# Kernel tuning notes

Hardware: AMD Instinct MI355X
Metric: run time of the kernel (lower is better)

Reference implementation:

```python
import jax, jax.numpy as jnp
import numpy as np

D_EMBED = 384
D_FF = 64
TAU = 0.1
T0, T1 = 0.0, 1.0
N_STEPS = 10


def setup_inputs() -> dict:
    key = jax.random.key(0)
    ks = jax.random.split(key, 6)
    B, n, d, f = 64, 1024, D_EMBED, D_FF
    init = lambda k, sh, fan: (jax.random.normal(k, sh, jnp.float32) / np.sqrt(fan)).astype(jnp.float32)
    return {
        "embeddings": jax.random.normal(ks[0], (B, n, d), jnp.float32),
        "W1": init(ks[1], (d + 1, f), d + 1), "b1": jnp.zeros((f,), jnp.float32),
        "W2": init(ks[2], (f, f), f),       "b2": jnp.zeros((f,), jnp.float32),
        "W3": init(ks[3], (f, d), f),       "b3": jnp.zeros((d,), jnp.float32),
        "Ws": init(ks[4], (d, 1), d),       "bs": jnp.zeros((1,), jnp.float32),
    }


def reference(embeddings, W1, b1, W2, b2, W3, b3, Ws, bs):
    B, n, d = embeddings.shape
    h0 = embeddings.reshape(B * n, d)
    dt = (T1 - T0) / N_STEPS

    def ode_f(t, h):
        # time-aware dynamics: concat scalar t to hidden state
        t_col = jnp.full((h.shape[0], 1), t, dtype=h.dtype)
        x = jnp.concatenate([h, t_col], axis=-1)
        x = jnp.tanh(x @ W1 + b1)
        x = jnp.tanh(x @ W2 + b2)
        return x @ W3 + b3

    def rk4_step(h, t):
        k1 = ode_f(t, h)
        k2 = ode_f(t + dt * 0.5, h + (dt * 0.5) * k1)
        k3 = ode_f(t + dt * 0.5, h + (dt * 0.5) * k2)
        k4 = ode_f(t + dt, h + dt * k3)
        return h + (dt / 6.0) * (k1 + 2.0 * k2 + 2.0 * k3 + k4), None

    ts = T0 + dt * jnp.arange(N_STEPS, dtype=jnp.float32)
    h_final, _ = jax.lax.scan(rk4_step, h0, ts)
    h_final = h_final.reshape(B, n, d)

    scores = (h_final @ Ws + bs).squeeze(-1)  # (B, n)

    # NeuralSort (Grover et al.): P_hat = softmax((C - A@1@1^T)^T / tau)
    s_col = scores[:, :, None]                        # (B, n, 1)
    A = jnp.abs(s_col - scores[:, None, :])           # (B, n, n) pairwise |s_i - s_j|
    row_sum = jnp.sum(A, axis=-1, keepdims=True)      # A @ one one^T, broadcast over cols
    scaling = (n + 1 - 2.0 * (jnp.arange(n, dtype=scores.dtype) + 1.0))  # (n,)
    C = s_col * scaling[None, None, :]                # C[b,i,j] = s_i * scaling_j
    P_max = jnp.transpose(C - row_sum, (0, 2, 1))
    P_hat = jax.nn.softmax(P_max / TAU, axis=-1)      # (B, n, n) soft permutation

    x_sorted = jnp.einsum('bij,bjd->bid', P_hat, embeddings)
    return x_sorted, scores
```

## Files before the change

### kernel.cpp

```cpp
#include <hip/hip_runtime.h>
#include <hip/hip_bf16.h>

#define NT 1024
#define DD 384
#define FF 64

typedef __attribute__((ext_vector_type(8))) _Float16 half8;
typedef __attribute__((ext_vector_type(4))) float f32x4;
typedef __attribute__((ext_vector_type(4))) unsigned uint32x4;

#define LO_SCALE 2048.f
#define INV2048  4.8828125e-4f

__device__ __forceinline__ float tanh_fast(float x){
    x = fminf(fmaxf(x, -15.f), 15.f);
    float e = __expf(2.f*x);
    return (e - 1.f) * __builtin_amdgcn_rcpf(e + 1.f);
}

__device__ __forceinline__ unsigned short h2u(_Float16 h){ return __builtin_bit_cast(unsigned short, h); }

__device__ __forceinline__ unsigned short split2_comp(float x, int comp){
    _Float16 hi = (_Float16)x;
    if (comp == 0) return h2u(hi);
    float r = (x - (float)hi) * LO_SCALE;
    _Float16 lo = (_Float16)r;
    return h2u(lo);
}

__device__ __forceinline__ void split_pack4(const float* v, unsigned* ph, unsigned* pl){
#pragma unroll
    for (int p=0;p<2;++p){
        float a=v[2*p], b=v[2*p+1];
        _Float16 ha=(_Float16)a, hb=(_Float16)b;
        ph[p] = (unsigned)h2u(ha) | ((unsigned)h2u(hb)<<16);
        float ra=(a-(float)ha)*LO_SCALE, rb=(b-(float)hb)*LO_SCALE;
        pl[p] = __builtin_bit_cast(unsigned, __builtin_amdgcn_cvt_pkrtz(ra, rb));
    }
}

__global__ void k_prep(const float* __restrict__ W1, const float* __restrict__ W2,
                       const float* __restrict__ W3, unsigned short* __restrict__ F)
{
    unsigned short* W1F = F;
    unsigned short* W2F = F + 49152;
    unsigned short* W3F = F + 57344;
    const int t = blockIdx.x*256 + threadIdx.x;
    const int NTH = gridDim.x*256;
    for (int i=t; i<49152; i+=NTH){
        int j=i&7, l=(i>>3)&63, u=i>>9;
        int kb=u%12, v=u/12, mb=v&3, comp=v>>2;
        int k=kb*32+8*(l>>4)+j, c=mb*16+(l&15);
        W1F[i] = split2_comp(W1[k*64+c], comp);
    }
    for (int i=t; i<8192; i+=NTH){
        int j=i&7, l=(i>>3)&63, u=i>>9;
        int kb=u&1, v=u>>1, mb=v&3, comp=v>>2;
        int k=kb*32+8*(l>>4)+j, c=mb*16+(l&15);
        W2F[i] = split2_comp(W2[k*64+c], comp);
    }
    for (int i=t; i<49152; i+=NTH){
        int j=i&7, l=(i>>3)&63, u=i>>9;
        int kb=u&1, v=u>>1, mb=v%24, comp=v/24;
        int k=kb*32+8*(l>>4)+j, c=mb*16+(l&15);
        W3F[i] = split2_comp(W3[k*384+c], comp);
    }
}

__global__ void k_prepE(const float* __restrict__ emb, unsigned short* __restrict__ EF)
{
    __shared__ float tile[32][388];
    const int b   = blockIdx.x >> 5;
    const int kb  = blockIdx.x & 31;
    const int tid = threadIdx.x;
    const float* src = emb + ((long long)b*NT + kb*32)*DD;
    for (int o = tid; o < 32*96; o += 256){
        int r = o/96, c4 = (o%96)*4;
        *(float4*)&tile[r][c4] = *(const float4*)&src[r*384 + c4];
    }
    __syncthreads();
    unsigned short* dst = EF + ((long long)b*24*32 + kb)*512;
    for (int o = tid; o < 24*512; o += 256){
        int mb = o >> 9, q = o & 511;
        int l = q >> 3, jj = q & 7;
        float v = tile[8*(l>>4)+jj][mb*16 + (l&15)];
        dst[(long long)mb*16384 + q] = h2u((_Float16)v);
    }
}

#define MFMA3(AH,AL,BH,BL,ACC,ACC2) do{ \
    ACC  = __builtin_amdgcn_mfma_f32_16x16x32_f16(AH,BH,ACC,0,0,0); \
    ACC2 = __builtin_amdgcn_mfma_f32_16x16x32_f16(AH,BL,ACC2,0,0,0); \
    ACC2 = __builtin_amdgcn_mfma_f32_16x16x32_f16(AL,BH,ACC2,0,0,0); \
}while(0)

struct AF { half8 h, l; };
#define LDA(P, CS) AF{ *(const half8*)(P), *(const half8*)((P)+(CS)) }
#define LDB(BASE, KB) do{ \
    bh = *(const half8*)((BASE) + (KB)*2048); \
    bl = *(const half8*)((BASE) + (KB)*2048 + 1024); \
}while(0)

__global__ __launch_bounds__(512) __attribute__((amdgpu_waves_per_eu(2,2)))
void k_ode(const float* __restrict__ emb,
           const float* __restrict__ W1,
           const float* __restrict__ b1, const float* __restrict__ b2,
           const float* __restrict__ b3, const float* __restrict__ Ws,
           const float* __restrict__ bs,
           const unsigned short* __restrict__ W1F,
           const unsigned short* __restrict__ W2F,
           const unsigned short* __restrict__ W3F,
           float* __restrict__ scores)
{
    extern __shared__ char smem[];
    unsigned short* hf  = (unsigned short*)smem;
    unsigned short* x1f = hf  + 24576;
    unsigned short* x2f = x1f + 4096;
    float*          red = (float*)(x2f + 4096);
    float*          h0l = red + 512;

    unsigned* hf32  = (unsigned*)hf;
    unsigned* x1f32 = (unsigned*)x1f;
    unsigned* x2f32 = (unsigned*)x2f;

    const int tid  = threadIdx.x;
    const int lane = tid & 63;
    const int w    = __builtin_amdgcn_readfirstlane(tid >> 6);
    const int g    = lane >> 4;
    const int rr   = lane & 15;
    const int nb   = w & 1;
    const int mbA  = w >> 1;
    const int rowl = nb*16 + rr;
    const long long row0 = (long long)blockIdx.x * 32;
    const float dt = 0.1f;

    const unsigned short* hrd  = hf  + nb*512 + lane*8;
    const unsigned short* x1rd = x1f + nb*512 + lane*8;
    const unsigned short* x2rd = x2f + nb*512 + lane*8;
    const unsigned wxp = nb*256 + rr*4 + 2*(g&1);
    const unsigned wx1 = ((unsigned)(mbA>>1))*1024 + 64u*((2*mbA+(g>>1))&3) + wxp;
    const int h0base = rowl*388 + mbA*96 + 4*g;

    float arc[24];
#pragma unroll
    for (int t=0;t<6;++t){
        f32x4 v = *(const f32x4*)(emb + (row0+rowl)*DD + mbA*96 + t*16 + 4*g);
        float hw[4] = {v[0],v[1],v[2],v[3]};
        *(float4*)(h0l + h0base + 16*t) = make_float4(hw[0],hw[1],hw[2],hw[3]);
        unsigned ph[2],pl[2];
        split_pack4(hw,ph,pl);
        const unsigned wh = ((unsigned)((6*mbA+t)>>1))*1024 + 64u*((2*t+(g>>1))&3) + wxp;
        *(uint2*)(hf32 + wh       ) = make_uint2(ph[0],ph[1]);
        *(uint2*)(hf32 + wh +  512) = make_uint2(pl[0],pl[1]);
    }

#define M3SEC(T, ACC, ACC2) do{ \
    ACC2 = (f32x4){0.f,0.f,0.f,0.f}; \
    const unsigned short* A3 = W3F + (unsigned)((6*mbA+(T))*2)*512 + lane*8; \
    AF w0 = LDA(A3, 24576); \
    AF w1 = LDA(A3+512, 24576); \
    MFMA3(w0.h,w0.l,B0h,B0l,ACC,ACC2); \
    MFMA3(w1.h,w1.l,B1h,B1l,ACC,ACC2); \
    __builtin_amdgcn_sched_barrier(0); \
}while(0)

#define M3UPD(T, ACC, ACC2) do{ \
    f32x4 h0v = *(const f32x4*)(h0l + h0base + 16*(T)); \
    float hw[4]; \
    if (stage < 3){ \
        _Pragma("unroll") \
        for (int r=0;r<4;++r){ float kr=fmaf(ACC2[r], INV2048, ACC[r]); \
            arc[4*(T)+r] = fmaf(wacc, kr, arc[4*(T)+r]); \
            hw[r] = fmaf(cs, kr, h0v[r]); } \
    } else { \
        _Pragma("unroll") \
        for (int r=0;r<4;++r){ float kr=fmaf(ACC2[r], INV2048, ACC[r]); \
            arc[4*(T)+r] = fmaf(wacc, kr, arc[4*(T)+r]); \
            hw[r] = h0v[r] + arc[4*(T)+r]; } \
        *(float4*)(h0l + h0base + 16*(T)) = make_float4(hw[0],hw[1],hw[2],hw[3]); \
    } \
    unsigned ph[2],pl[2]; \
    split_pack4(hw,ph,pl); \
    const unsigned wh = ((unsigned)((6*mbA+(T))>>1))*1024 + 64u*((2*(T)+(g>>1))&3) + wxp; \
    *(uint2*)(hf32 + wh       ) = make_uint2(ph[0],ph[1]); \
    *(uint2*)(hf32 + wh +  512) = make_uint2(pl[0],pl[1]); \
}while(0)

#pragma unroll 1
    for (int step=0; step<10; ++step){
        const float tstep = dt*(float)step;
#pragma unroll
        for (int j=0;j<24;++j) arc[j]=0.f;

#pragma unroll 1
        for (int stage=0; stage<4; ++stage){
            const float ts = tstep + ((stage==0)?0.f:((stage==3)?dt:0.5f*dt));
            __syncthreads();

            f32x4 accA, accB, accLA, accLB;
            {
                f32x4 b1v = *(const f32x4*)(b1 + mbA*16 + 4*g);
                f32x4 wtv = *(const f32x4*)(W1 + 384*64 + mbA*16 + 4*g);
#pragma unroll
                for (int r=0;r<4;++r){ accA[r] = fmaf(ts, wtv[r], b1v[r]); accB[r] = 0.f; accLA[r] = 0.f; accLB[r] = 0.f; }
            }
            {
                const unsigned short* A1 = W1F + mbA*6144 + lane*8;
                AF a0 = LDA(A1, 24576);
                half8 bh0 = *(const half8*)(hrd);
                half8 bl0 = *(const half8*)(hrd + 1024);
#pragma unroll 1
                for (int p=0;p<6;++p){
                    AF a1 = LDA(A1 + (2*p+1)*512, 24576);
                    half8 bh1 = *(const half8*)(hrd + (2*p+1)*2048);
                    half8 bl1 = *(const half8*)(hrd + (2*p+1)*2048 + 1024);
                    MFMA3(a0.h,a0.l,bh0,bl0,accA,accLA);
                    const int kbn = (p<5) ? (2*p+2) : 0;
                    a0 = LDA(A1 + kbn*512, 24576);
                    bh0 = *(const half8*)(hrd + kbn*2048);
                    bl0 = *(const half8*)(hrd + kbn*2048 + 1024);
                    MFMA3(a1.h,a1.l,bh1,bl1,accB,accLB);
                }
            }
            {
                float xv[4];
#pragma unroll
                for (int r=0;r<4;++r) xv[r] = tanh_fast(accA[r] + accB[r] + (accLA[r]+accLB[r])*INV2048);
                unsigned ph[2],pl[2];
                split_pack4(xv,ph,pl);
                *(uint2*)(x1f32 + wx1       ) = make_uint2(ph[0],ph[1]);
                *(uint2*)(x1f32 + wx1 +  512) = make_uint2(pl[0],pl[1]);
            }
            __syncthreads();

            f32x4 acc2 = *(const f32x4*)(b2 + mbA*16 + 4*g);
            f32x4 acc2L;
            {
#pragma unroll
                for (int r=0;r<4;++r) acc2L[r] = 0.f;
                const unsigned short* A2 = W2F + mbA*1024 + lane*8;
                AF c0 = LDA(A2, 4096);
                AF c1 = LDA(A2 + 512, 4096);
                half8 bh,bl;
                LDB(x1rd, 0);
                MFMA3(c0.h,c0.l,bh,bl,acc2,acc2L);
                LDB(x1rd, 1);
                MFMA3(c1.h,c1.l,bh,bl,acc2,acc2L);
            }
            {
                float xv[4];
#pragma unroll
                for (int r=0;r<4;++r) xv[r] = tanh_fast(acc2[r] + acc2L[r]*INV2048);
                unsigned ph[2],pl[2];
                split_pack4(xv,ph,pl);
                *(uint2*)(x2f32 + wx1       ) = make_uint2(ph[0],ph[1]);
                *(uint2*)(x2f32 + wx1 +  512) = make_uint2(pl[0],pl[1]);
            }
            __syncthreads();

            const float wacc = (dt/6.f)*((stage==1||stage==2)?2.f:1.f);
            const float cs   = (stage==2)?dt:0.5f*dt;
            {
                half8 B0h = *(const half8*)(x2rd);
                half8 B0l = *(const half8*)(x2rd + 1024);
                half8 B1h = *(const half8*)(x2rd + 2048);
                half8 B1l = *(const half8*)(x2rd + 3072);
                f32x4 ac0 = *(const f32x4*)(b3 + mbA*96       + 4*g);
                f32x4 ac1 = *(const f32x4*)(b3 + mbA*96 + 16  + 4*g);
                f32x4 ac2b = *(const f32x4*)(b3 + mbA*96 + 32 + 4*g);
                f32x4 ac3 = *(const f32x4*)(b3 + mbA*96 + 48  + 4*g);
                f32x4 ac4 = *(const f32x4*)(b3 + mbA*96 + 64  + 4*g);
                f32x4 ac5 = *(const f32x4*)(b3 + mbA*96 + 80  + 4*g);
                f32x4 c0,c1,c2,c3,c4,c5;
                M3SEC(0, ac0, c0);
                M3SEC(1, ac1, c1);   M3UPD(0, ac0, c0);
                M3SEC(2, ac2b, c2);  M3UPD(1, ac1, c1);
                M3SEC(3, ac3, c3);   M3UPD(2, ac2b, c2);
                M3SEC(4, ac4, c4);   M3UPD(3, ac3, c3);
                M3SEC(5, ac5, c5);   M3UPD(4, ac4, c4);
                M3UPD(5, ac5, c5);
            }
        }
    }

    float part = 0.f;
#pragma unroll
    for (int t=0;t<6;++t){
        f32x4 hv  = *(const f32x4*)(h0l + h0base + 16*t);
        f32x4 wsv = *(const f32x4*)(Ws + mbA*96 + t*16 + 4*g);
#pragma unroll
        for (int r=0;r<4;++r) part = fmaf(hv[r], wsv[r], part);
    }
    __syncthreads();
    red[rowl*16 + mbA*4 + g] = part;
    __syncthreads();
    if (tid < 32){
        float s = bs[0];
#pragma unroll
        for (int q=0;q<16;++q) s += red[tid*16+q];
        scores[row0 + tid] = s;
    }
#undef M3SEC
#undef M3UPD
}

__global__ void k_rowsum(const float* __restrict__ scores, float* __restrict__ rs)
{
    __shared__ float s[NT];
    const int b   = blockIdx.x >> 2;
    const int q   = blockIdx.x & 3;
    const int tid = threadIdx.x;
    for (int i=tid; i<NT; i+=256) s[i] = scores[b*NT + i];
    __syncthreads();
    const int i = q*256 + tid;
    const float si = s[i];
    float sum = 0.f;
#pragma unroll 8
    for (int j=0; j<NT; ++j) sum += fabsf(si - s[j]);
    rs[b*NT + i] = sum;
}

__global__ __launch_bounds__(512)
void k_pvm(const unsigned short* __restrict__ EF, const float* __restrict__ scores,
           const float* __restrict__ rs, float* __restrict__ out)
{
    __shared__ float s_tr[2*NT];
    __shared__ float red_m[16][33];
    __shared__ float red_s[16][33];
    __shared__ float s_MI[64];

    const int tid = threadIdx.x;
    const int b   = blockIdx.x >> 5;
    const int j0  = (blockIdx.x & 31) * 32;
    const float invT2 = 10.f * 1.44269504f;

    for (int i = tid; i < NT; i += 512){
        s_tr[2*i  ] =  scores[b*NT + i] * invT2;
        s_tr[2*i+1] = -rs[b*NT + i] * invT2;
    }
    __syncthreads();

    {
        const int jl = tid & 31;
        const int ch = tid >> 5;
        const float SC = 1023.f - 2.f*(float)(j0 + jl);
        const int ib = ch*64;
        float m = -3.0e38f;
#pragma unroll 4
        for (int i = ib; i < ib+64; ++i)
            m = fmaxf(m, fmaf(s_tr[2*i], SC, s_tr[2*i+1]));
        float sum = 0.f;
#pragma unroll 4
        for (int i = ib; i < ib+64; ++i)
            sum += exp2f(fmaf(s_tr[2*i], SC, s_tr[2*i+1]) - m);
        red_m[ch][jl] = m; red_s[ch][jl] = sum;
    }
    __syncthreads();
    if (tid < 32){
        float M = -3.0e38f;
#pragma unroll
        for (int c=0;c<16;++c) M = fmaxf(M, red_m[c][tid]);
        float S = 0.f;
#pragma unroll
        for (int c=0;c<16;++c) S += red_s[c][tid] * exp2f(red_m[c][tid] - M);
        s_MI[tid]    = M;
        s_MI[32+tid] = __builtin_amdgcn_rcpf(S);
    }
    __syncthreads();

    const int lane = tid & 63;
    const int w    = __builtin_amdgcn_readfirstlane(tid >> 6);
    const int g    = lane >> 4;
    const int rr   = lane & 15;
    const int nb   = w & 1;
    const int mbA  = w >> 1;
    const int jl   = nb*16 + rr;
    const float SCv = 1023.f - 2.f*(float)(j0 + jl);
    const float Mv  = s_MI[jl];
    const float Iv  = s_MI[32 + jl];

    f32x4 ac0={0,0,0,0}, ac1={0,0,0,0}, ac2={0,0,0,0},
          ac3={0,0,0,0}, ac4={0,0,0,0}, ac5={0,0,0,0};

    const unsigned short* Abase = EF + (((long long)b*24 + mbA*6)*32)*512 + lane*8;

#pragma unroll 2
    for (int kb = 0; kb < 32; ++kb){
        const float* str = s_tr + 2*(kb*32 + 8*g);
        uint32x4 pw;
#pragma unroll
        for (int p=0;p<4;++p){
            float L0 = fmaf(str[4*p  ], SCv, str[4*p+1]) - Mv;
            float L1 = fmaf(str[4*p+2], SCv, str[4*p+3]) - Mv;
            pw[p] = __builtin_bit_cast(unsigned,
                        __builtin_amdgcn_cvt_pkrtz(exp2f(L0), exp2f(L1)));
        }
        half8 Pf = __builtin_bit_cast(half8, pw);
        const unsigned short* A = Abase + kb*512;
        ac0 = __builtin_amdgcn_mfma_f32_16x16x32_f16(*(const half8*)(A          ), Pf, ac0, 0,0,0);
        ac1 = __builtin_amdgcn_mfma_f32_16x16x32_f16(*(const half8*)(A + 16384  ), Pf, ac1, 0,0,0);
        ac2 = __builtin_amdgcn_mfma_f32_16x16x32_f16(*(const half8*)(A + 2*16384), Pf, ac2, 0,0,0);
        ac3 = __builtin_amdgcn_mfma_f32_16x16x32_f16(*(const half8*)(A + 3*16384), Pf, ac3, 0,0,0);
        ac4 = __builtin_amdgcn_mfma_f32_16x16x32_f16(*(const half8*)(A + 4*16384), Pf, ac4, 0,0,0);
        ac5 = __builtin_amdgcn_mfma_f32_16x16x32_f16(*(const half8*)(A + 5*16384), Pf, ac5, 0,0,0);
    }

    float* op = out + ((long long)b*NT + j0 + jl)*DD + mbA*96 + 4*g;
    *(float4*)(op       ) = make_float4(ac0[0]*Iv, ac0[1]*Iv, ac0[2]*Iv, ac0[3]*Iv);
    *(float4*)(op + 16  ) = make_float4(ac1[0]*Iv, ac1[1]*Iv, ac1[2]*Iv, ac1[3]*Iv);
    *(float4*)(op + 32  ) = make_float4(ac2[0]*Iv, ac2[1]*Iv, ac2[2]*Iv, ac2[3]*Iv);
    *(float4*)(op + 48  ) = make_float4(ac3[0]*Iv, ac3[1]*Iv, ac3[2]*Iv, ac3[3]*Iv);
    *(float4*)(op + 64  ) = make_float4(ac4[0]*Iv, ac4[1]*Iv, ac4[2]*Iv, ac4[3]*Iv);
    *(float4*)(op + 80  ) = make_float4(ac5[0]*Iv, ac5[1]*Iv, ac5[2]*Iv, ac5[3]*Iv);
}

__global__ __launch_bounds__(256, 2)
void k_pv(const float* __restrict__ emb, const float* __restrict__ scores,
          const float* __restrict__ rs, float* __restrict__ out)
{
    __shared__ float s_tt[NT];
    __shared__ float s_rp[NT];
    __shared__ float red_m[8][33];
    __shared__ float red_s[8][33];
    __shared__ float s_M[32], s_I[32];

    const int tid = threadIdx.x;
    const int b   = blockIdx.x >> 5;
    const int j0  = (blockIdx.x & 31) * 32;
    const float invT = 10.f;

    for (int i=tid; i<NT; i+=256){
        s_tt[i] =  scores[b*NT + i] * invT;
        s_rp[i] = -rs[b*NT + i] * invT;
    }
    __syncthreads();
    {
        const int jl = tid & 31;
        const int ch = tid >> 5;
        const float SC = 1023.f - 2.f*(float)(j0 + jl);
        const int ibeg = ch*128;
        float m = -3.0e38f;
#pragma unroll 4
        for (int i=ibeg; i<ibeg+128; ++i){
            float L = fmaf(s_tt[i], SC, s_rp[i]);
            m = fmaxf(m, L);
        }
        float sum = 0.f;
#pragma unroll 4
        for (int i=ibeg; i<ibeg+128; ++i){
            float L = fmaf(s_tt[i], SC, s_rp[i]);
            sum += __expf(L - m);
        }
        red_m[ch][jl] = m; red_s[ch][jl] = sum;
    }
    __syncthreads();
    if (tid < 32){
        float M = -3.0e38f;
#pragma unroll
        for (int c=0; c<8; ++c) M = fmaxf(M, red_m[c][tid]);
        float S = 0.f;
#pragma unroll
        for (int c=0; c<8; ++c) S += red_s[c][tid]*__expf(red_m[c][tid]-M);
        s_M[tid] = M;
        s_I[tid] = 1.f/S;
    }
    __syncthreads();

    const int tx = tid & 31;
    const int jy = tid >> 5;
    float accv[4][12];
#pragma unroll
    for (int v=0; v<4; ++v)
#pragma unroll
        for (int u=0; u<12; ++u) accv[v][u] = 0.f;

    float SCv[4], Mv[4], Iv[4];
#pragma unroll
    for (int v=0; v<4; ++v){
        const int jl = jy + 8*v;
        SCv[v] = 1023.f - 2.f*(float)(j0 + jl);
        Mv[v]  = s_M[jl];
        Iv[v]  = s_I[jl];
    }
    const float* ep = emb + ((long long)b*NT)*DD + tx;
#pragma unroll 2
    for (int i=0; i<NT; ++i){
        const float ti = s_tt[i], ri = s_rp[i];
        float ev[12];
#pragma unroll
        for (int u=0; u<12; ++u) ev[u] = ep[(long long)i*DD + 32*u];
        float p[4];
#pragma unroll
        for (int v=0; v<4; ++v)
            p[v] = __expf(fmaf(ti, SCv[v], ri) - Mv[v]);
#pragma unroll
        for (int v=0; v<4; ++v)
#pragma unroll
            for (int u=0; u<12; ++u) accv[v][u] = fmaf(p[v], ev[u], accv[v][u]);
    }
#pragma unroll
    for (int v=0; v<4; ++v){
        float* op = out + ((long long)b*NT + j0 + jy + 8*v)*DD + tx;
#pragma unroll
        for (int u=0; u<12; ++u) op[32*u] = accv[v][u]*Iv[v];
    }
}

extern "C" void kernel_launch(void* const* d_in, const int* in_sizes, int n_in,
                              void* d_out, int out_size, void* d_ws, size_t ws_size,
                              hipStream_t stream)
{
    const float* emb = (const float*)d_in[0];
    const float* W1  = (const float*)d_in[1];
    const float* b1  = (const float*)d_in[2];
    const float* W2  = (const float*)d_in[3];
    const float* b2  = (const float*)d_in[4];
    const float* W3  = (const float*)d_in[5];
    const float* b3  = (const float*)d_in[6];
    const float* Ws  = (const float*)d_in[7];
    const float* bs  = (const float*)d_in[8];

    const int B = in_sizes[0] / (NT*DD);
    float* out    = (float*)d_out;
    float* scores = out + (long long)B*NT*DD;

    unsigned short* WF = (unsigned short*)d_ws;
    const unsigned short* W1F = WF;
    const unsigned short* W2F = WF + 49152;
    const unsigned short* W3F = WF + 57344;
    float* rsum = (float*)((char*)d_ws + 319488);

    const size_t efOff = 589824;
    const size_t efBytes = (size_t)B*24*32*512*2;
    const bool useMFMApv = (ws_size >= efOff + efBytes);
    unsigned short* EF = (unsigned short*)((char*)d_ws + efOff);

    const int ODE_LDS = 117248;
    hipFuncSetAttribute(reinterpret_cast<const void*>(k_ode),
                        hipFuncAttributeMaxDynamicSharedMemorySize, ODE_LDS);

    hipLaunchKernelGGL(k_prep, dim3(64), dim3(256), 0, stream, W1, W2, W3, WF);
    if (useMFMApv)
        hipLaunchKernelGGL(k_prepE, dim3(B*32), dim3(256), 0, stream, emb, EF);
    hipLaunchKernelGGL(k_ode, dim3(B*NT/32), dim3(512), ODE_LDS, stream,
                       emb, W1, b1, b2, b3, Ws, bs, W1F, W2F, W3F, scores);
    hipLaunchKernelGGL(k_rowsum, dim3(B*4), dim3(256), 0, stream, scores, rsum);
    if (useMFMApv)
        hipLaunchKernelGGL(k_pvm, dim3(B*32), dim3(512), 0, stream, EF, scores, rsum, out);
    else
        hipLaunchKernelGGL(k_pv, dim3(B*32), dim3(256), 0, stream, emb, scores, rsum, out);
}
```

Baseline: 1.404 ms.

## Double ODE block rows to 64 with 1024 threads and keep state in registers

The ODE kernel now processes 64 rows per block with 16 waves instead of 32 rows with 8, so each W1/W2/W3 fragment loaded from global memory is reused across twice as many rows. The fp32 hidden state h0 moves from LDS into per-thread registers, which frees LDS for the larger fp16 hi/lo tiles. The reduction buffer is aliased onto x1f, and the b3 loads move into the MFMA section macro. The waves_per_eu hint is dropped, so register pressure at 1024 threads may cause spills, and the 128KB of LDS allows only one block per CU.

```diff
diff --git a/kernel.cpp b/kernel.cpp
--- a/kernel.cpp
+++ b/kernel.cpp
@@ -97,11 +97,11 @@
 struct AF { half8 h, l; };
 #define LDA(P, CS) AF{ *(const half8*)(P), *(const half8*)((P)+(CS)) }
 #define LDB(BASE, KB) do{ \
-    bh = *(const half8*)((BASE) + (KB)*2048); \
-    bl = *(const half8*)((BASE) + (KB)*2048 + 1024); \
+    bh = *(const half8*)((BASE) + (KB)*4096); \
+    bl = *(const half8*)((BASE) + (KB)*4096 + 2048); \
 }while(0)
 
-__global__ __launch_bounds__(512) __attribute__((amdgpu_waves_per_eu(2,2)))
+__global__ __launch_bounds__(1024)
 void k_ode(const float* __restrict__ emb,
            const float* __restrict__ W1,
            const float* __restrict__ b1, const float* __restrict__ b2,
@@ -114,10 +114,8 @@
 {
     extern __shared__ char smem[];
     unsigned short* hf  = (unsigned short*)smem;
-    unsigned short* x1f = hf  + 24576;
-    unsigned short* x2f = x1f + 4096;
-    float*          red = (float*)(x2f + 4096);
-    float*          h0l = red + 512;
+    unsigned short* x1f = hf  + 49152;
+    unsigned short* x2f = x1f + 8192;
 
     unsigned* hf32  = (unsigned*)hf;
     unsigned* x1f32 = (unsigned*)x1f;
@@ -128,33 +126,35 @@
     const int w    = __builtin_amdgcn_readfirstlane(tid >> 6);
     const int g    = lane >> 4;
     const int rr   = lane & 15;
-    const int nb   = w & 1;
-    const int mbA  = w >> 1;
+    const int nb   = w & 3;
+    const int mbA  = w >> 2;
     const int rowl = nb*16 + rr;
-    const long long row0 = (long long)blockIdx.x * 32;
+    const long long row0 = (long long)blockIdx.x * 64;
     const float dt = 0.1f;
 
     const unsigned short* hrd  = hf  + nb*512 + lane*8;
     const unsigned short* x1rd = x1f + nb*512 + lane*8;
     const unsigned short* x2rd = x2f + nb*512 + lane*8;
     const unsigned wxp = nb*256 + rr*4 + 2*(g&1);
-    const unsigned wx1 = ((unsigned)(mbA>>1))*1024 + 64u*((2*mbA+(g>>1))&3) + wxp;
-    const int h0base = rowl*388 + mbA*96 + 4*g;
-
+    const unsigned wx1 = ((unsigned)(mbA>>1))*2048 + 64u*((2*mbA+(g>>1))&3) + wxp;
+
+    float h0r[24];
     float arc[24];
 #pragma unroll
     for (int t=0;t<6;++t){
         f32x4 v = *(const f32x4*)(emb + (row0+rowl)*DD + mbA*96 + t*16 + 4*g);
         float hw[4] = {v[0],v[1],v[2],v[3]};
-        *(float4*)(h0l + h0base + 16*t) = make_float4(hw[0],hw[1],hw[2],hw[3]);
+#pragma unroll
+        for (int r=0;r<4;++r) h0r[4*t+r] = hw[r];
         unsigned ph[2],pl[2];
         split_pack4(hw,ph,pl);
-        const unsigned wh = ((unsigned)((6*mbA+t)>>1))*1024 + 64u*((2*t+(g>>1))&3) + wxp;
-        *(uint2*)(hf32 + wh       ) = make_uint2(ph[0],ph[1]);
-        *(uint2*)(hf32 + wh +  512) = make_uint2(pl[0],pl[1]);
+        const unsigned wh = ((unsigned)((6*mbA+t)>>1))*2048 + 64u*((2*t+(g>>1))&3) + wxp;
+        *(uint2*)(hf32 + wh        ) = make_uint2(ph[0],ph[1]);
+        *(uint2*)(hf32 + wh + 1024 ) = make_uint2(pl[0],pl[1]);
     }
 
 #define M3SEC(T, ACC, ACC2) do{ \
+    ACC = *(const f32x4*)(b3 + mbA*96 + 16*(T) + 4*g); \
     ACC2 = (f32x4){0.f,0.f,0.f,0.f}; \
     const unsigned short* A3 = W3F + (unsigned)((6*mbA+(T))*2)*512 + lane*8; \
     AF w0 = LDA(A3, 24576); \
@@ -165,25 +165,24 @@
 }while(0)
 
 #define M3UPD(T, ACC, ACC2) do{ \
-    f32x4 h0v = *(const f32x4*)(h0l + h0base + 16*(T)); \
     float hw[4]; \
     if (stage < 3){ \
         _Pragma("unroll") \
         for (int r=0;r<4;++r){ float kr=fmaf(ACC2[r], INV2048, ACC[r]); \
             arc[4*(T)+r] = fmaf(wacc, kr, arc[4*(T)+r]); \
-            hw[r] = fmaf(cs, kr, h0v[r]); } \
+            hw[r] = fmaf(cs, kr, h0r[4*(T)+r]); } \
     } else { \
         _Pragma("unroll") \
         for (int r=0;r<4;++r){ float kr=fmaf(ACC2[r], INV2048, ACC[r]); \
             arc[4*(T)+r] = fmaf(wacc, kr, arc[4*(T)+r]); \
-            hw[r] = h0v[r] + arc[4*(T)+r]; } \
-        *(float4*)(h0l + h0base + 16*(T)) = make_float4(hw[0],hw[1],hw[2],hw[3]); \
+            hw[r] = h0r[4*(T)+r] + arc[4*(T)+r]; \
+            h0r[4*(T)+r] = hw[r]; } \
     } \
     unsigned ph[2],pl[2]; \
     split_pack4(hw,ph,pl); \
-    const unsigned wh = ((unsigned)((6*mbA+(T))>>1))*1024 + 64u*((2*(T)+(g>>1))&3) + wxp; \
-    *(uint2*)(hf32 + wh       ) = make_uint2(ph[0],ph[1]); \
-    *(uint2*)(hf32 + wh +  512) = make_uint2(pl[0],pl[1]); \
+    const unsigned wh = ((unsigned)((6*mbA+(T))>>1))*2048 + 64u*((2*(T)+(g>>1))&3) + wxp; \
+    *(uint2*)(hf32 + wh        ) = make_uint2(ph[0],ph[1]); \
+    *(uint2*)(hf32 + wh + 1024 ) = make_uint2(pl[0],pl[1]); \
 }while(0)
 
 #pragma unroll 1
@@ -207,19 +206,16 @@
             {
                 const unsigned short* A1 = W1F + mbA*6144 + lane*8;
                 AF a0 = LDA(A1, 24576);
-                half8 bh0 = *(const half8*)(hrd);
-                half8 bl0 = *(const half8*)(hrd + 1024);
 #pragma unroll 1
                 for (int p=0;p<6;++p){
                     AF a1 = LDA(A1 + (2*p+1)*512, 24576);
-                    half8 bh1 = *(const half8*)(hrd + (2*p+1)*2048);
-                    half8 bl1 = *(const half8*)(hrd + (2*p+1)*2048 + 1024);
-                    MFMA3(a0.h,a0.l,bh0,bl0,accA,accLA);
+                    half8 bh,bl;
+                    LDB(hrd, 2*p);
+                    MFMA3(a0.h,a0.l,bh,bl,accA,accLA);
                     const int kbn = (p<5) ? (2*p+2) : 0;
                     a0 = LDA(A1 + kbn*512, 24576);
-                    bh0 = *(const half8*)(hrd + kbn*2048);
-                    bl0 = *(const half8*)(hrd + kbn*2048 + 1024);
-                    MFMA3(a1.h,a1.l,bh1,bl1,accB,accLB);
+                    LDB(hrd, 2*p+1);
+                    MFMA3(a1.h,a1.l,bh,bl,accB,accLB);
                 }
             }
             {
@@ -228,8 +224,8 @@
                 for (int r=0;r<4;++r) xv[r] = tanh_fast(accA[r] + accB[r] + (accLA[r]+accLB[r])*INV2048);
                 unsigned ph[2],pl[2];
                 split_pack4(xv,ph,pl);
-                *(uint2*)(x1f32 + wx1       ) = make_uint2(ph[0],ph[1]);
-                *(uint2*)(x1f32 + wx1 +  512) = make_uint2(pl[0],pl[1]);
+                *(uint2*)(x1f32 + wx1        ) = make_uint2(ph[0],ph[1]);
+                *(uint2*)(x1f32 + wx1 + 1024 ) = make_uint2(pl[0],pl[1]);
             }
             __syncthreads();
 
@@ -253,8 +249,8 @@
                 for (int r=0;r<4;++r) xv[r] = tanh_fast(acc2[r] + acc2L[r]*INV2048);
                 unsigned ph[2],pl[2];
                 split_pack4(xv,ph,pl);
-                *(uint2*)(x2f32 + wx1       ) = make_uint2(ph[0],ph[1]);
-                *(uint2*)(x2f32 + wx1 +  512) = make_uint2(pl[0],pl[1]);
+                *(uint2*)(x2f32 + wx1        ) = make_uint2(ph[0],ph[1]);
+                *(uint2*)(x2f32 + wx1 + 1024 ) = make_uint2(pl[0],pl[1]);
             }
             __syncthreads();
 
@@ -262,15 +258,10 @@
             const float cs   = (stage==2)?dt:0.5f*dt;
             {
                 half8 B0h = *(const half8*)(x2rd);
-                half8 B0l = *(const half8*)(x2rd + 1024);
-                half8 B1h = *(const half8*)(x2rd + 2048);
-                half8 B1l = *(const half8*)(x2rd + 3072);
-                f32x4 ac0 = *(const f32x4*)(b3 + mbA*96       + 4*g);
-                f32x4 ac1 = *(const f32x4*)(b3 + mbA*96 + 16  + 4*g);
-                f32x4 ac2b = *(const f32x4*)(b3 + mbA*96 + 32 + 4*g);
-                f32x4 ac3 = *(const f32x4*)(b3 + mbA*96 + 48  + 4*g);
-                f32x4 ac4 = *(const f32x4*)(b3 + mbA*96 + 64  + 4*g);
-                f32x4 ac5 = *(const f32x4*)(b3 + mbA*96 + 80  + 4*g);
+                half8 B0l = *(const half8*)(x2rd + 2048);
+                half8 B1h = *(const half8*)(x2rd + 4096);
+                half8 B1l = *(const half8*)(x2rd + 6144);
+                f32x4 ac0,ac1,ac2b,ac3,ac4,ac5;
                 f32x4 c0,c1,c2,c3,c4,c5;
                 M3SEC(0, ac0, c0);
                 M3SEC(1, ac1, c1);   M3UPD(0, ac0, c0);
@@ -286,15 +277,15 @@
     float part = 0.f;
 #pragma unroll
     for (int t=0;t<6;++t){
-        f32x4 hv  = *(const f32x4*)(h0l + h0base + 16*t);
         f32x4 wsv = *(const f32x4*)(Ws + mbA*96 + t*16 + 4*g);
 #pragma unroll
-        for (int r=0;r<4;++r) part = fmaf(hv[r], wsv[r], part);
-    }
-    __syncthreads();
+        for (int r=0;r<4;++r) part = fmaf(h0r[4*t+r], wsv[r], part);
+    }
+    __syncthreads();
+    float* red = (float*)x1f;
     red[rowl*16 + mbA*4 + g] = part;
     __syncthreads();
-    if (tid < 32){
+    if (tid < 64){
         float s = bs[0];
 #pragma unroll
         for (int q=0;q<16;++q) s += red[tid*16+q];
@@ -535,14 +526,14 @@
     const bool useMFMApv = (ws_size >= efOff + efBytes);
     unsigned short* EF = (unsigned short*)((char*)d_ws + efOff);
 
-    const int ODE_LDS = 117248;
+    const int ODE_LDS = 131072;
     hipFuncSetAttribute(reinterpret_cast<const void*>(k_ode),
                         hipFuncAttributeMaxDynamicSharedMemorySize, ODE_LDS);
 
     hipLaunchKernelGGL(k_prep, dim3(64), dim3(256), 0, stream, W1, W2, W3, WF);
     if (useMFMApv)
         hipLaunchKernelGGL(k_prepE, dim3(B*32), dim3(256), 0, stream, emb, EF);
-    hipLaunchKernelGGL(k_ode, dim3(B*NT/32), dim3(512), ODE_LDS, stream,
+    hipLaunchKernelGGL(k_ode, dim3(B*NT/64), dim3(1024), ODE_LDS, stream,
                        emb, W1, b1, b2, b3, Ws, bs, W1F, W2F, W3F, scores);
     hipLaunchKernelGGL(k_rowsum, dim3(B*4), dim3(256), 0, stream, scores, rsum);
     if (useMFMApv)
```

After: 4.058 ms. 189% more time.

## Stage W1 high halves in LDS and keep one h0 slice in registers

Applied to the files above, without the earlier changes.

Copies the fp16 high parts of W1 into shared memory at kernel start, so the first GEMM reads them from LDS and fetches only the low parts from global/cache. To free LDS, one of six h0 slices is kept in registers instead of shared memory, and the reduction buffer reuses x1f. The b3 bias loads are moved into the per-section macro. LDS grows to about 156KB per block, which holds occupancy at one 512-thread block per CU and may add register pressure.

```diff
diff --git a/kernel.cpp b/kernel.cpp
--- a/kernel.cpp
+++ b/kernel.cpp
@@ -116,8 +116,8 @@
     unsigned short* hf  = (unsigned short*)smem;
     unsigned short* x1f = hf  + 24576;
     unsigned short* x2f = x1f + 4096;
-    float*          red = (float*)(x2f + 4096);
-    float*          h0l = red + 512;
+    unsigned short* w1h = x2f + 4096;
+    float*          h0l = (float*)(smem + 114688);
 
     unsigned* hf32  = (unsigned*)hf;
     unsigned* x1f32 = (unsigned*)x1f;
@@ -134,19 +134,30 @@
     const long long row0 = (long long)blockIdx.x * 32;
     const float dt = 0.1f;
 
+    {
+        const unsigned* srcw = (const unsigned*)W1F;
+        unsigned* dstw = (unsigned*)w1h;
+        for (int o = tid; o < 12288; o += 512) dstw[o] = srcw[o];
+    }
+
     const unsigned short* hrd  = hf  + nb*512 + lane*8;
     const unsigned short* x1rd = x1f + nb*512 + lane*8;
     const unsigned short* x2rd = x2f + nb*512 + lane*8;
     const unsigned wxp = nb*256 + rr*4 + 2*(g&1);
     const unsigned wx1 = ((unsigned)(mbA>>1))*1024 + 64u*((2*mbA+(g>>1))&3) + wxp;
-    const int h0base = rowl*388 + mbA*96 + 4*g;
+    const int h0base = rowl*324 + mbA*80 + 4*g;
+    float h0r5[4];
 
     float arc[24];
 #pragma unroll
     for (int t=0;t<6;++t){
         f32x4 v = *(const f32x4*)(emb + (row0+rowl)*DD + mbA*96 + t*16 + 4*g);
         float hw[4] = {v[0],v[1],v[2],v[3]};
-        *(float4*)(h0l + h0base + 16*t) = make_float4(hw[0],hw[1],hw[2],hw[3]);
+        if (t < 5) *(float4*)(h0l + h0base + 16*t) = make_float4(hw[0],hw[1],hw[2],hw[3]);
+        else {
+#pragma unroll
+            for (int r=0;r<4;++r) h0r5[r] = hw[r];
+        }
         unsigned ph[2],pl[2];
         split_pack4(hw,ph,pl);
         const unsigned wh = ((unsigned)((6*mbA+t)>>1))*1024 + 64u*((2*t+(g>>1))&3) + wxp;
@@ -155,6 +166,7 @@
     }
 
 #define M3SEC(T, ACC, ACC2) do{ \
+    ACC = *(const f32x4*)(b3 + mbA*96 + 16*(T) + 4*g); \
     ACC2 = (f32x4){0.f,0.f,0.f,0.f}; \
     const unsigned short* A3 = W3F + (unsigned)((6*mbA+(T))*2)*512 + lane*8; \
     AF w0 = LDA(A3, 24576); \
@@ -165,7 +177,14 @@
 }while(0)
 
 #define M3UPD(T, ACC, ACC2) do{ \
-    f32x4 h0v = *(const f32x4*)(h0l + h0base + 16*(T)); \
+    float h0v[4]; \
+    if ((T) < 5){ \
+        f32x4 _hv = *(const f32x4*)(h0l + h0base + 16*(T)); \
+        h0v[0]=_hv[0]; h0v[1]=_hv[1]; h0v[2]=_hv[2]; h0v[3]=_hv[3]; \
+    } else { \
+        _Pragma("unroll") \
+        for (int r=0;r<4;++r) h0v[r] = h0r5[r]; \
+    } \
     float hw[4]; \
     if (stage < 3){ \
         _Pragma("unroll") \
@@ -177,7 +196,11 @@
         for (int r=0;r<4;++r){ float kr=fmaf(ACC2[r], INV2048, ACC[r]); \
             arc[4*(T)+r] = fmaf(wacc, kr, arc[4*(T)+r]); \
             hw[r] = h0v[r] + arc[4*(T)+r]; } \
-        *(float4*)(h0l + h0base + 16*(T)) = make_float4(hw[0],hw[1],hw[2],hw[3]); \
+        if ((T) < 5) *(float4*)(h0l + h0base + 16*(T)) = make_float4(hw[0],hw[1],hw[2],hw[3]); \
+        else { \
+            _Pragma("unroll") \
+            for (int r=0;r<4;++r) h0r5[r] = hw[r]; \
+        } \
     } \
     unsigned ph[2],pl[2]; \
     split_pack4(hw,ph,pl); \
@@ -205,21 +228,23 @@
                 for (int r=0;r<4;++r){ accA[r] = fmaf(ts, wtv[r], b1v[r]); accB[r] = 0.f; accLA[r] = 0.f; accLB[r] = 0.f; }
             }
             {
-                const unsigned short* A1 = W1F + mbA*6144 + lane*8;
-                AF a0 = LDA(A1, 24576);
-                half8 bh0 = *(const half8*)(hrd);
-                half8 bl0 = *(const half8*)(hrd + 1024);
+                const unsigned short* H1 = w1h + mbA*6144 + lane*8;
+                const unsigned short* L1 = W1F + 24576 + mbA*6144 + lane*8;
+                half8 l0 = *(const half8*)(L1);
+                half8 l1 = *(const half8*)(L1 + 512);
 #pragma unroll 1
                 for (int p=0;p<6;++p){
-                    AF a1 = LDA(A1 + (2*p+1)*512, 24576);
-                    half8 bh1 = *(const half8*)(hrd + (2*p+1)*2048);
-                    half8 bl1 = *(const half8*)(hrd + (2*p+1)*2048 + 1024);
-                    MFMA3(a0.h,a0.l,bh0,bl0,accA,accLA);
-                    const int kbn = (p<5) ? (2*p+2) : 0;
-                    a0 = LDA(A1 + kbn*512, 24576);
-                    bh0 = *(const half8*)(hrd + kbn*2048);
-                    bl0 = *(const half8*)(hrd + kbn*2048 + 1024);
-                    MFMA3(a1.h,a1.l,bh1,bl1,accB,accLB);
+                    half8 hh0 = *(const half8*)(H1 + (2*p)*512);
+                    half8 hh1 = *(const half8*)(H1 + (2*p+1)*512);
+                    const int kb2 = (p<5) ? (2*p+2) : 0;
+                    half8 nl0 = *(const half8*)(L1 + kb2*512);
+                    half8 nl1 = *(const half8*)(L1 + (kb2+1)*512);
+                    half8 bh,bl;
+                    LDB(hrd, 2*p);
+                    MFMA3(hh0,l0,bh,bl,accA,accLA);
+                    LDB(hrd, 2*p+1);
+                    MFMA3(hh1,l1,bh,bl,accB,accLB);
+                    l0 = nl0; l1 = nl1;
                 }
             }
             {
@@ -265,12 +290,7 @@
                 half8 B0l = *(const half8*)(x2rd + 1024);
                 half8 B1h = *(const half8*)(x2rd + 2048);
                 half8 B1l = *(const half8*)(x2rd + 3072);
-                f32x4 ac0 = *(const f32x4*)(b3 + mbA*96       + 4*g);
-                f32x4 ac1 = *(const f32x4*)(b3 + mbA*96 + 16  + 4*g);
-                f32x4 ac2b = *(const f32x4*)(b3 + mbA*96 + 32 + 4*g);
-                f32x4 ac3 = *(const f32x4*)(b3 + mbA*96 + 48  + 4*g);
-                f32x4 ac4 = *(const f32x4*)(b3 + mbA*96 + 64  + 4*g);
-                f32x4 ac5 = *(const f32x4*)(b3 + mbA*96 + 80  + 4*g);
+                f32x4 ac0,ac1,ac2b,ac3,ac4,ac5;
                 f32x4 c0,c1,c2,c3,c4,c5;
                 M3SEC(0, ac0, c0);
                 M3SEC(1, ac1, c1);   M3UPD(0, ac0, c0);
@@ -286,12 +306,20 @@
     float part = 0.f;
 #pragma unroll
     for (int t=0;t<6;++t){
-        f32x4 hv  = *(const f32x4*)(h0l + h0base + 16*t);
+        float hv[4];
+        if (t < 5){
+            f32x4 _hv = *(const f32x4*)(h0l + h0base + 16*t);
+            hv[0]=_hv[0]; hv[1]=_hv[1]; hv[2]=_hv[2]; hv[3]=_hv[3];
+        } else {
+#pragma unroll
+            for (int r=0;r<4;++r) hv[r] = h0r5[r];
+        }
         f32x4 wsv = *(const f32x4*)(Ws + mbA*96 + t*16 + 4*g);
 #pragma unroll
         for (int r=0;r<4;++r) part = fmaf(hv[r], wsv[r], part);
     }
     __syncthreads();
+    float* red = (float*)x1f;
     red[rowl*16 + mbA*4 + g] = part;
     __syncthreads();
     if (tid < 32){
@@ -535,7 +563,7 @@
     const bool useMFMApv = (ws_size >= efOff + efBytes);
     unsigned short* EF = (unsigned short*)((char*)d_ws + efOff);
 
-    const int ODE_LDS = 117248;
+    const int ODE_LDS = 156160;
     hipFuncSetAttribute(reinterpret_cast<const void*>(k_ode),
                         hipFuncAttributeMaxDynamicSharedMemorySize, ODE_LDS);
 
```

Result: faster. 1.322 ms (-5.8%).
